# Kernel optimization log

Measured on AMD Instinct MI355X. Metric: run time of the kernel, lower is better.

Reference implementation:

```python
import itertools
import jax, jax.numpy as jnp
import numpy as np

EPS = 1e-15
B, K, H, W = 64, 8, 128, 128


def setup_inputs() -> dict:
    key = jax.random.key(0)
    k1, k2 = jax.random.split(key)
    pred_masks = jax.random.uniform(k1, (B, K, H, W), dtype=jnp.float32)
    aug_masks = jax.random.uniform(k2, (B, K, H, W), dtype=jnp.float32)
    return {"pred_masks": pred_masks, "aug_masks": aug_masks}


def _mask_kl_div(pred, true):
    # true * (log(true+eps) - log(pred+eps)), mean over (H, W)
    return (true * (jnp.log(true + EPS) - jnp.log(pred + EPS))).mean(axis=(-2, -1))


# all K! permutations, precomputed once (K=8 -> 40320 perms)
_PERMS = jnp.asarray(np.array(list(itertools.permutations(range(K))), dtype=np.int32))


def reference(pred_masks, aug_masks):
    b, k, h, w = pred_masks.shape
    t = aug_masks  # targets are detached in torch for the cost matrix
    # Fused pairwise KL cost matrix (avoids the (B,K,K,H,W) broadcast):
    # C[b,i,j] = mean_hw[ t_j*log(t_j+eps) ] - mean_hw[ t_j*log(p_i+eps) ]
    ent = (t * jnp.log(t + EPS)).mean(axis=(-2, -1))          # (B, K) over j
    cross = jnp.einsum('bjhw,bihw->bij', t, jnp.log(pred_masks + EPS)) / (h * w)
    C = ent[:, None, :] - cross                                # (B, K, K)
    # exact linear assignment via exhaustive search over K! permutations
    rows = jnp.arange(k)
    costs = C[:, rows[None, :], _PERMS].sum(axis=-1)           # (B, K!)
    R2C = _PERMS[jnp.argmin(costs, axis=1)]                    # (B, K) col for each row
    # permute rows: out[b, i] = pred[b, argsort(R2C)[b, i]]
    row_perm = jnp.argsort(R2C, axis=1)
    pred_perm = jnp.take_along_axis(pred_masks, row_perm[:, :, None, None], axis=1)
    l = _mask_kl_div(pred_perm, t)                             # (B, K)
    return l.mean(), pred_perm[..., None]
```

## Files before the change

### kernel.cpp

```cpp
#include <hip/hip_runtime.h>


#define BB 64
#define KK 8
#define HW 16384
#define CH 16
#define CHUNK 1024
#define EPSF 1e-15f

struct MaskTab {
    unsigned char masks[255];
    int off[9];
};

constexpr MaskTab make_tab() {
    MaskTab t{};
    int idx = 0;
    for (int p = 1; p <= 8; ++p) {
        t.off[p - 1] = idx;
        for (int m = 1; m < 256; ++m) {
            int c = 0;
            for (int b = 0; b < 8; ++b) c += (m >> b) & 1;
            if (c == p) t.masks[idx++] = (unsigned char)m;
        }
    }
    t.off[8] = idx;
    return t;
}

__constant__ MaskTab kTab = make_tab();

__device__ __forceinline__ float dot4(float4 t, float4 l) {
    return t.x * l.x + t.y * l.y + t.z * l.z + t.w * l.w;
}

__device__ __forceinline__ float4 log4(float4 a) {
    float4 r;
    r.x = __logf(a.x + EPSF); r.y = __logf(a.y + EPSF);
    r.z = __logf(a.z + EPSF); r.w = __logf(a.w + EPSF);
    return r;
}

__global__ __launch_bounds__(256) void cost_kernel(const float* __restrict__ pred,
                                                   const float* __restrict__ aug,
                                                   float* __restrict__ part)
{
    const int blk   = blockIdx.x;
    const int b     = blk >> 4;
    const int chunk = blk & 15;
    const int tid   = threadIdx.x;
    const int wave  = tid >> 6;
    const int lane  = tid & 63;
    const int w2    = 2 * wave;

    const float* p0 = pred + (size_t)b * (KK * HW) + (size_t)w2 * HW + chunk * CHUNK;
    const float* p1 = p0 + HW;
    const float* tb = aug + (size_t)b * (KK * HW) + chunk * CHUNK;

    float acc[16];
#pragma unroll
    for (int v = 0; v < 16; ++v) acc[v] = 0.f;
    float e0 = 0.f, e1 = 0.f;

#pragma unroll
    for (int it = 0; it < 4; ++it) {
        const int off = it * 256 + lane * 4;

        float4 la = log4(*(const float4*)(p0 + off));
        float4 lc = log4(*(const float4*)(p1 + off));

#pragma unroll
        for (int j = 0; j < 8; ++j) {
            float4 t4 = *(const float4*)(tb + (size_t)j * HW + off);
            acc[j]     += dot4(t4, la);
            acc[8 + j] += dot4(t4, lc);
            if (j == w2) {
                e0 += dot4(t4, log4(t4));
            } else if (j == w2 + 1) {
                e1 += dot4(t4, log4(t4));
            }
        }
    }

#pragma unroll
    for (int v = 0; v < 16; ++v) {
        float s = acc[v];
#pragma unroll
        for (int d = 1; d < 64; d <<= 1) s += __shfl_xor(s, d);
        acc[v] = s;
    }
#pragma unroll
    for (int d = 1; d < 64; d <<= 1) e0 += __shfl_xor(e0, d);
#pragma unroll
    for (int d = 1; d < 64; d <<= 1) e1 += __shfl_xor(e1, d);

    if (lane == 0) {
        float* dst = part + (size_t)blk * 72;
#pragma unroll
        for (int j = 0; j < 8; ++j) {
            dst[16 * wave + j]     = acc[j];
            dst[16 * wave + 8 + j] = acc[8 + j];
        }
        dst[64 + w2]     = e0;
        dst[64 + w2 + 1] = e1;
    }
}

__global__ __launch_bounds__(256) void permute_kernel(const float* __restrict__ pred,
                                                      const float* __restrict__ part,
                                                      float* __restrict__ out)
{
    __shared__ float red[72];
    __shared__ float C[64];
    __shared__ float dp[256];
    __shared__ int   choice[256];
    __shared__ int   inv8[8];

    const int g    = blockIdx.x;
    const int p    = g >> 1;
    const int half = g & 1;
    const int b    = p >> 3;
    const int tid  = threadIdx.x;

    const float* pb = part + (size_t)b * CH * 72;
    if (tid < 72) {
        float s = 0.f;
#pragma unroll
        for (int c = 0; c < CH; ++c) s += pb[c * 72 + tid];
        red[tid] = s;
    }
    __syncthreads();
    if (tid < 64) C[tid] = red[64 + (tid & 7)] - red[tid];
    if (tid == 0) dp[0] = 0.f;
    __syncthreads();

    const int grp = tid >> 3;
    const int j   = tid & 7;

    for (int lvl = 1; lvl <= 8; ++lvl) {
        const int start = kTab.off[lvl - 1];
        const int end   = kTab.off[lvl];
        const float* Crow = &C[(lvl - 1) * 8];
        for (int base = start; base < end; base += 32) {
            const int mi = base + grp;
            if (mi < end) {
                const int M = kTab.masks[mi];
                float v  = 1e30f;
                int   bj = 0;
                if (M & (1 << j)) {
                    v  = dp[M ^ (1 << j)] + Crow[j];
                    bj = j;
                }
#pragma unroll
                for (int d = 1; d < 8; d <<= 1) {
                    float ov = __shfl_xor(v, d);
                    int   oj = __shfl_xor(bj, d);
                    if (ov < v) { v = ov; bj = oj; }
                }
                if (j == 0) { dp[M] = v; choice[M] = bj; }
            }
        }
        __syncthreads();
    }

    if (tid == 0) {
        int mask = 255;
        for (int r = 7; r >= 0; --r) {
            const int jj = choice[mask];
            inv8[jj] = r;
            mask ^= 1 << jj;
        }
        if (g == (b << 4))
            atomicAdd(out, dp[255] * (1.0f / (16384.0f * 512.0f)));
    }
    __syncthreads();

    const int src_row = inv8[p & 7];
    const float* src = pred + ((size_t)(b << 3) + src_row) * HW;
    float*       drow = out + 1 + (size_t)p * HW;

#pragma unroll
    for (int m = 0; m < 8; ++m) {
        const int f = half * 2048 + tid + 256 * m;
        const int e = 3 + 4 * f;
        if (f < 4095) {
            float4 v;
            v.x = src[e]; v.y = src[e + 1]; v.z = src[e + 2]; v.w = src[e + 3];
            *(float4*)(drow + e) = v;
        } else {
            drow[0] = src[0]; drow[1] = src[1]; drow[2] = src[2];
            drow[16383] = src[16383];
        }
    }
}

extern "C" void kernel_launch(void* const* d_in, const int* in_sizes, int n_in,
                              void* d_out, int out_size, void* d_ws, size_t ws_size,
                              hipStream_t stream) {
    const float* pred = (const float*)d_in[0];
    const float* aug  = (const float*)d_in[1];
    float* out = (float*)d_out;
    float* part = (float*)d_ws;

    hipMemsetAsync(d_out, 0, sizeof(float), stream);

    cost_kernel<<<dim3(BB * CH), dim3(256), 0, stream>>>(pred, aug, part);
    permute_kernel<<<dim3(1024), dim3(256), 0, stream>>>(pred, part, out);
}
```

Measured before the change: 123.3 us.

## Stage cost-kernel inputs in LDS via global_load_lds with finer chunks

The cost kernel now splits each batch into 64 smaller chunks of 256 elements instead of 16 chunks of 1024, launching four times as many blocks. Each block loads all 8 pred and 8 aug rows for its chunk directly into shared memory with global_load_lds. Waves then read their target tiles from LDS, so the 4x redundant global reads of aug across waves go away and more blocks are in flight. In exchange, the partial buffer grows and the permute kernel must sum 64 partials per batch. The permute kernel's loop uses the CH macro, so it picks up the new count without other edits.

```diff
diff --git a/kernel.cpp b/kernel.cpp
--- a/kernel.cpp
+++ b/kernel.cpp
@@ -4,8 +4,8 @@
 #define BB 64
 #define KK 8
 #define HW 16384
-#define CH 16
-#define CHUNK 1024
+#define CH 64
+#define CHUNK 256
 #define EPSF 1e-15f
 
 struct MaskTab {
@@ -45,41 +45,47 @@
                                                    const float* __restrict__ aug,
                                                    float* __restrict__ part)
 {
+    __shared__ float tile[16][CHUNK];
+
     const int blk   = blockIdx.x;
-    const int b     = blk >> 4;
-    const int chunk = blk & 15;
+    const int b     = blk >> 6;
+    const int chunk = blk & 63;
     const int tid   = threadIdx.x;
     const int wave  = tid >> 6;
     const int lane  = tid & 63;
-    const int w2    = 2 * wave;
-
-    const float* p0 = pred + (size_t)b * (KK * HW) + (size_t)w2 * HW + chunk * CHUNK;
-    const float* p1 = p0 + HW;
-    const float* tb = aug + (size_t)b * (KK * HW) + chunk * CHUNK;
+
+    const size_t base = (size_t)b * (KK * HW) + (size_t)chunk * CHUNK;
+
+#pragma unroll
+    for (int m = 0; m < 4; ++m) {
+        const int vr = wave + 4 * m;
+        const float* g = ((vr < 8) ? (pred + base + (size_t)vr * HW)
+                                   : (aug  + base + (size_t)(vr - 8) * HW)) + lane * 4;
+        __builtin_amdgcn_global_load_lds(
+            (const __attribute__((address_space(1))) void*)g,
+            (__attribute__((address_space(3))) void*)&tile[vr][lane * 4],
+            16, 0, 0);
+    }
+    __syncthreads();
+
+    const int w2 = 2 * wave;
+    const int e4 = lane * 4;
+
+    const float4 p0 = *(const float4*)&tile[w2][e4];
+    const float4 p1 = *(const float4*)&tile[w2 + 1][e4];
+    const float4 la = log4(p0);
+    const float4 lc = log4(p1);
+    const float4 t0 = *(const float4*)&tile[8 + w2][e4];
+    const float4 t1 = *(const float4*)&tile[8 + w2 + 1][e4];
+    float e0 = dot4(t0, log4(t0));
+    float e1 = dot4(t1, log4(t1));
 
     float acc[16];
 #pragma unroll
-    for (int v = 0; v < 16; ++v) acc[v] = 0.f;
-    float e0 = 0.f, e1 = 0.f;
-
-#pragma unroll
-    for (int it = 0; it < 4; ++it) {
-        const int off = it * 256 + lane * 4;
-
-        float4 la = log4(*(const float4*)(p0 + off));
-        float4 lc = log4(*(const float4*)(p1 + off));
-
-#pragma unroll
-        for (int j = 0; j < 8; ++j) {
-            float4 t4 = *(const float4*)(tb + (size_t)j * HW + off);
-            acc[j]     += dot4(t4, la);
-            acc[8 + j] += dot4(t4, lc);
-            if (j == w2) {
-                e0 += dot4(t4, log4(t4));
-            } else if (j == w2 + 1) {
-                e1 += dot4(t4, log4(t4));
-            }
-        }
+    for (int j = 0; j < 8; ++j) {
+        const float4 tv = *(const float4*)&tile[8 + j][e4];
+        acc[j]     = dot4(tv, la);
+        acc[8 + j] = dot4(tv, lc);
     }
 
 #pragma unroll
```

After: 129.6 us. 1.05x slower.

## Move assignment DP into last-arriving cost block; prefetch loads; slim permute kernel

Applied to the files above, without the earlier changes.

The cost kernel now covers 2048-element spans per block (512 blocks) and software-pipelines its loads by fetching the next chunk while computing on the current one. The last block to finish for each batch, detected with an atomic counter, reduces the partials and runs the subset DP, then writes the inverse permutation and per-batch loss to workspace. The permute kernel becomes a pure copy over 2048 blocks, and one block sums the losses, so the output memset is no longer needed. The aim is to stop every copy block from redoing the partial reduction and DP, at the cost of a fence/atomic tail, fewer cost blocks, and more registers.

```diff
diff --git a/kernel.cpp b/kernel.cpp
--- a/kernel.cpp
+++ b/kernel.cpp
@@ -4,8 +4,8 @@
 #define BB 64
 #define KK 8
 #define HW 16384
-#define CH 16
-#define CHUNK 1024
+#define SPANS 8
+#define SPAN 2048
 #define EPSF 1e-15f
 
 struct MaskTab {
@@ -41,53 +41,78 @@
     return r;
 }
 
+struct Chunk {
+    float4 p0, p1;
+    float4 t[8];
+};
+
+__device__ __forceinline__ Chunk ldchunk(const float* __restrict__ p0,
+                                         const float* __restrict__ p1,
+                                         const float* __restrict__ tb, int off) {
+    Chunk c;
+    c.p0 = *(const float4*)(p0 + off);
+    c.p1 = *(const float4*)(p1 + off);
+#pragma unroll
+    for (int j = 0; j < 8; ++j) c.t[j] = *(const float4*)(tb + j * HW + off);
+    return c;
+}
+
 __global__ __launch_bounds__(256) void cost_kernel(const float* __restrict__ pred,
                                                    const float* __restrict__ aug,
-                                                   float* __restrict__ part)
+                                                   float* __restrict__ part,
+                                                   int* __restrict__ ctr,
+                                                   int* __restrict__ ws_inv,
+                                                   float* __restrict__ ws_loss)
 {
-    const int blk   = blockIdx.x;
-    const int b     = blk >> 4;
-    const int chunk = blk & 15;
-    const int tid   = threadIdx.x;
-    const int wave  = tid >> 6;
-    const int lane  = tid & 63;
-    const int w2    = 2 * wave;
-
-    const float* p0 = pred + (size_t)b * (KK * HW) + (size_t)w2 * HW + chunk * CHUNK;
+    __shared__ float C[64];
+    __shared__ float dp[256];
+    __shared__ int   choice[256];
+    __shared__ int   lastf;
+
+    const int blk  = blockIdx.x;
+    const int b    = blk >> 3;
+    const int s    = blk & 7;
+    const int tid  = threadIdx.x;
+    const int lane = tid & 63;
+    const int w2   = __builtin_amdgcn_readfirstlane(2 * (tid >> 6));
+    const int wave = w2 >> 1;
+
+    const size_t base = (size_t)b * (KK * HW) + (size_t)s * SPAN;
+    const float* p0 = pred + base + (size_t)w2 * HW;
     const float* p1 = p0 + HW;
-    const float* tb = aug + (size_t)b * (KK * HW) + chunk * CHUNK;
+    const float* tb = aug + base;
+    const int l4 = lane * 4;
 
     float acc[16];
 #pragma unroll
     for (int v = 0; v < 16; ++v) acc[v] = 0.f;
     float e0 = 0.f, e1 = 0.f;
 
-#pragma unroll
-    for (int it = 0; it < 4; ++it) {
-        const int off = it * 256 + lane * 4;
-
-        float4 la = log4(*(const float4*)(p0 + off));
-        float4 lc = log4(*(const float4*)(p1 + off));
-
+    Chunk cur = ldchunk(p0, p1, tb, l4);
+#pragma unroll
+    for (int c = 0; c < 8; ++c) {
+        Chunk nxt;
+        if (c < 7) nxt = ldchunk(p0, p1, tb, (c + 1) * 256 + l4);
+
+        const float4 la = log4(cur.p0);
+        const float4 lc = log4(cur.p1);
 #pragma unroll
         for (int j = 0; j < 8; ++j) {
-            float4 t4 = *(const float4*)(tb + (size_t)j * HW + off);
-            acc[j]     += dot4(t4, la);
-            acc[8 + j] += dot4(t4, lc);
-            if (j == w2) {
-                e0 += dot4(t4, log4(t4));
-            } else if (j == w2 + 1) {
-                e1 += dot4(t4, log4(t4));
-            }
-        }
+            const float4 tv = cur.t[j];
+            acc[j]     += dot4(tv, la);
+            acc[8 + j] += dot4(tv, lc);
+            if (j == w2)     e0 += dot4(tv, log4(tv));
+            if (j == w2 + 1) e1 += dot4(tv, log4(tv));
+        }
+        if (c < 7) cur = nxt;
     }
 
 #pragma unroll
     for (int v = 0; v < 16; ++v) {
-        float s = acc[v];
-#pragma unroll
-        for (int d = 1; d < 64; d <<= 1) s += __shfl_xor(s, d);
-        acc[v] = s;
+        float sv = acc[v];
+#pragma unroll
+        for (int d = 1; d < 64; d <<= 1) sv += __shfl_xor(sv, d);
+        acc[v] = sv;
     }
 #pragma unroll
     for (int d = 1; d < 64; d <<= 1) e0 += __shfl_xor(e0, d);
@@ -104,45 +129,41 @@
         dst[64 + w2]     = e0;
         dst[64 + w2 + 1] = e1;
     }
-}
-
-__global__ __launch_bounds__(256) void permute_kernel(const float* __restrict__ pred,
-                                                      const float* __restrict__ part,
-                                                      float* __restrict__ out)
-{
-    __shared__ float red[72];
-    __shared__ float C[64];
-    __shared__ float dp[256];
-    __shared__ int   choice[256];
-    __shared__ int   inv8[8];
-
-    const int g    = blockIdx.x;
-    const int p    = g >> 1;
-    const int half = g & 1;
-    const int b    = p >> 3;
-    const int tid  = threadIdx.x;
-
-    const float* pb = part + (size_t)b * CH * 72;
-    if (tid < 72) {
-        float s = 0.f;
-#pragma unroll
-        for (int c = 0; c < CH; ++c) s += pb[c * 72 + tid];
-        red[tid] = s;
-    }
+
     __syncthreads();
-    if (tid < 64) C[tid] = red[64 + (tid & 7)] - red[tid];
+    if (tid == 0) {
+        __threadfence();
+        const int old = atomicAdd(&ctr[b], 1);
+        lastf = (old == SPANS - 1) ? 1 : 0;
+    }
+    __syncthreads();
+    if (!lastf) return;
+    __threadfence();
+
+    if (tid < 64) {
+        const float* pb = part + (size_t)(b * 8) * 72;
+        float ssum = 0.f;
+#pragma unroll
+        for (int s8 = 0; s8 < 8; ++s8) ssum += pb[s8 * 72 + tid];
+        float e = 0.f;
+        if (tid < 8) {
+#pragma unroll
+            for (int s8 = 0; s8 < 8; ++s8) e += pb[s8 * 72 + 64 + tid];
+        }
+        const float entj = __shfl(e, tid & 7);
+        C[tid] = entj - ssum;
+    }
     if (tid == 0) dp[0] = 0.f;
     __syncthreads();
 
     const int grp = tid >> 3;
     const int j   = tid & 7;
-
     for (int lvl = 1; lvl <= 8; ++lvl) {
         const int start = kTab.off[lvl - 1];
         const int end   = kTab.off[lvl];
         const float* Crow = &C[(lvl - 1) * 8];
-        for (int base = start; base < end; base += 32) {
-            const int mi = base + grp;
+        for (int bse = start; bse < end; bse += 32) {
+            const int mi = bse + grp;
             if (mi < end) {
                 const int M = kTab.masks[mi];
                 float v  = 1e30f;
@@ -153,8 +174,8 @@
                 }
 #pragma unroll
                 for (int d = 1; d < 8; d <<= 1) {
-                    float ov = __shfl_xor(v, d);
-                    int   oj = __shfl_xor(bj, d);
+                    const float ov = __shfl_xor(v, d);
+                    const int   oj = __shfl_xor(bj, d);
                     if (ov < v) { v = ov; bj = oj; }
                 }
                 if (j == 0) { dp[M] = v; choice[M] = bj; }
@@ -167,21 +188,31 @@
         int mask = 255;
         for (int r = 7; r >= 0; --r) {
             const int jj = choice[mask];
-            inv8[jj] = r;
+            ws_inv[b * 8 + jj] = r;
             mask ^= 1 << jj;
         }
-        if (g == (b << 4))
-            atomicAdd(out, dp[255] * (1.0f / (16384.0f * 512.0f)));
-    }
-    __syncthreads();
-
-    const int src_row = inv8[p & 7];
+        ws_loss[b] = dp[255] * (1.0f / (16384.0f * 512.0f));
+    }
+}
+
+__global__ __launch_bounds__(256) void permute_kernel(const float* __restrict__ pred,
+                                                      const int* __restrict__ ws_inv,
+                                                      const float* __restrict__ ws_loss,
+                                                      float* __restrict__ out)
+{
+    const int blk  = blockIdx.x;
+    const int pair = blk >> 2;
+    const int q    = blk & 3;
+    const int b    = pair >> 3;
+    const int tid  = threadIdx.x;
+
+    const int src_row = ws_inv[pair];
     const float* src = pred + ((size_t)(b << 3) + src_row) * HW;
-    float*       drow = out + 1 + (size_t)p * HW;
-
-#pragma unroll
-    for (int m = 0; m < 8; ++m) {
-        const int f = half * 2048 + tid + 256 * m;
+    float*      drow = out + 1 + (size_t)pair * HW;
+
+#pragma unroll
+    for (int m = 0; m < 4; ++m) {
+        const int f = q * 1024 + tid + 256 * m;
         const int e = 3 + 4 * f;
         if (f < 4095) {
             float4 v;
@@ -192,6 +223,13 @@
             drow[16383] = src[16383];
         }
     }
+
+    if (blk == 0 && tid < 64) {
+        float v = ws_loss[tid];
+#pragma unroll
+        for (int d = 1; d < 64; d <<= 1) v += __shfl_xor(v, d);
+        if (tid == 0) out[0] = v;
+    }
 }
 
 extern "C" void kernel_launch(void* const* d_in, const int* in_sizes, int n_in,
@@ -200,10 +238,14 @@
     const float* pred = (const float*)d_in[0];
     const float* aug  = (const float*)d_in[1];
     float* out = (float*)d_out;
-    float* part = (float*)d_ws;
-
-    hipMemsetAsync(d_out, 0, sizeof(float), stream);
-
-    cost_kernel<<<dim3(BB * CH), dim3(256), 0, stream>>>(pred, aug, part);
-    permute_kernel<<<dim3(1024), dim3(256), 0, stream>>>(pred, part, out);
-}
+
+    int*   ctr     = (int*)d_ws;
+    float* part    = (float*)d_ws + 64;
+    int*   ws_inv  = (int*)(part + 512 * 72);
+    float* ws_loss = (float*)(ws_inv + 512);
+
+    hipMemsetAsync(ctr, 0, 64 * sizeof(int), stream);
+
+    cost_kernel<<<dim3(BB * SPANS), dim3(256), 0, stream>>>(pred, aug, part, ctr, ws_inv, ws_loss);
+    permute_kernel<<<dim3(2048), dim3(256), 0, stream>>>(pred, ws_inv, ws_loss, out);
+}
```

Result: slower. 166.5 us (+35.1%).

## Double-buffer cost kernel loads into LDS via async global_load_lds and drop memset

Applied to the files above, without the earlier changes.

The cost kernel now streams pred and aug chunks into a double-buffered shared-memory tile using async global-to-LDS loads, prefetching the next chunk while computing on the current one. The separate hipMemsetAsync that zeroed the loss accumulator is replaced by a store from the first thread of cost_kernel, removing one launch. This adds 32KB LDS per block, which may reduce occupancy, and barriers per chunk; the data is still read once, so the gain depends on better latency hiding.

```diff
diff --git a/kernel.cpp b/kernel.cpp
--- a/kernel.cpp
+++ b/kernel.cpp
@@ -4,8 +4,10 @@
 #define BB 64
 #define KK 8
 #define HW 16384
-#define CH 16
-#define CHUNK 1024
+#define SPANS 16
+#define SPAN 1024
+#define NCH 4
+#define CHUNK 256
 #define EPSF 1e-15f
 
 struct MaskTab {
@@ -43,19 +45,40 @@
 
 __global__ __launch_bounds__(256) void cost_kernel(const float* __restrict__ pred,
                                                    const float* __restrict__ aug,
-                                                   float* __restrict__ part)
+                                                   float* __restrict__ part,
+                                                   float* __restrict__ out)
 {
-    const int blk   = blockIdx.x;
-    const int b     = blk >> 4;
-    const int chunk = blk & 15;
-    const int tid   = threadIdx.x;
-    const int wave  = tid >> 6;
-    const int lane  = tid & 63;
-    const int w2    = 2 * wave;
-
-    const float* p0 = pred + (size_t)b * (KK * HW) + (size_t)w2 * HW + chunk * CHUNK;
-    const float* p1 = p0 + HW;
-    const float* tb = aug + (size_t)b * (KK * HW) + chunk * CHUNK;
+    __shared__ float tile[2][16][CHUNK];
+
+    const int blk  = blockIdx.x;
+    const int b    = blk >> 4;
+    const int s    = blk & 15;
+    const int tid  = threadIdx.x;
+    const int wave = tid >> 6;
+    const int lane = tid & 63;
+
+    if (blk == 0 && tid == 0) out[0] = 0.f;
+
+    const size_t base = (size_t)b * (KK * HW) + (size_t)s * SPAN;
+    const int e4 = lane * 4;
+    const int w2 = 2 * wave;
+
+#define STAGE(c)                                                                          \
+    {                                                                                     \
+        const int pb_ = (c) & 1;                                                          \
+        _Pragma("unroll")                                                                 \
+        for (int m = 0; m < 4; ++m) {                                                     \
+            const int vr = wave + 4 * m;                                                  \
+            const float* g = ((vr < 8) ? (pred + base + (size_t)vr * HW)                  \
+                                       : (aug + base + (size_t)(vr - 8) * HW))            \
+                             + (c) * CHUNK + e4;                                          \
+            __builtin_amdgcn_global_load_lds(                                             \
+                (const __attribute__((address_space(1))) void*)g,                         \
+                (__attribute__((address_space(3))) void*)&tile[pb_][vr][e4], 16, 0, 0);   \
+        }                                                                                 \
+    }
+
+    STAGE(0)
 
     float acc[16];
 #pragma unroll
@@ -63,31 +86,30 @@
     float e0 = 0.f, e1 = 0.f;
 
 #pragma unroll
-    for (int it = 0; it < 4; ++it) {
-        const int off = it * 256 + lane * 4;
-
-        float4 la = log4(*(const float4*)(p0 + off));
-        float4 lc = log4(*(const float4*)(p1 + off));
-
+    for (int c = 0; c < NCH; ++c) {
+        __syncthreads();
+        if (c + 1 < NCH) STAGE(c + 1)
+
+        const int pb = c & 1;
+        const float4 la = log4(*(const float4*)&tile[pb][w2][e4]);
+        const float4 lc = log4(*(const float4*)&tile[pb][w2 + 1][e4]);
 #pragma unroll
         for (int j = 0; j < 8; ++j) {
-            float4 t4 = *(const float4*)(tb + (size_t)j * HW + off);
-            acc[j]     += dot4(t4, la);
-            acc[8 + j] += dot4(t4, lc);
-            if (j == w2) {
-                e0 += dot4(t4, log4(t4));
-            } else if (j == w2 + 1) {
-                e1 += dot4(t4, log4(t4));
-            }
-        }
-    }
+            const float4 tv = *(const float4*)&tile[pb][8 + j][e4];
+            acc[j]     += dot4(tv, la);
+            acc[8 + j] += dot4(tv, lc);
+            if (j == w2)     e0 += dot4(tv, log4(tv));
+            if (j == w2 + 1) e1 += dot4(tv, log4(tv));
+        }
+    }
+#undef STAGE
 
 #pragma unroll
     for (int v = 0; v < 16; ++v) {
-        float s = acc[v];
-#pragma unroll
-        for (int d = 1; d < 64; d <<= 1) s += __shfl_xor(s, d);
-        acc[v] = s;
+        float sv = acc[v];
+#pragma unroll
+        for (int d = 1; d < 64; d <<= 1) sv += __shfl_xor(sv, d);
+        acc[v] = sv;
     }
 #pragma unroll
     for (int d = 1; d < 64; d <<= 1) e0 += __shfl_xor(e0, d);
@@ -122,27 +144,26 @@
     const int b    = p >> 3;
     const int tid  = threadIdx.x;
 
-    const float* pb = part + (size_t)b * CH * 72;
+    const float* pb = part + (size_t)b * SPANS * 72;
     if (tid < 72) {
         float s = 0.f;
 #pragma unroll
-        for (int c = 0; c < CH; ++c) s += pb[c * 72 + tid];
+        for (int c = 0; c < SPANS; ++c) s += pb[c * 72 + tid];
         red[tid] = s;
     }
+    if (tid == 0) dp[0] = 0.f;
     __syncthreads();
     if (tid < 64) C[tid] = red[64 + (tid & 7)] - red[tid];
-    if (tid == 0) dp[0] = 0.f;
     __syncthreads();
 
     const int grp = tid >> 3;
     const int j   = tid & 7;
-
     for (int lvl = 1; lvl <= 8; ++lvl) {
         const int start = kTab.off[lvl - 1];
         const int end   = kTab.off[lvl];
         const float* Crow = &C[(lvl - 1) * 8];
-        for (int base = start; base < end; base += 32) {
-            const int mi = base + grp;
+        for (int bse = start; bse < end; bse += 32) {
+            const int mi = bse + grp;
             if (mi < end) {
                 const int M = kTab.masks[mi];
                 float v  = 1e30f;
@@ -153,8 +174,8 @@
                 }
 #pragma unroll
                 for (int d = 1; d < 8; d <<= 1) {
-                    float ov = __shfl_xor(v, d);
-                    int   oj = __shfl_xor(bj, d);
+                    const float ov = __shfl_xor(v, d);
+                    const int   oj = __shfl_xor(bj, d);
                     if (ov < v) { v = ov; bj = oj; }
                 }
                 if (j == 0) { dp[M] = v; choice[M] = bj; }
@@ -176,8 +197,8 @@
     __syncthreads();
 
     const int src_row = inv8[p & 7];
-    const float* src = pred + ((size_t)(b << 3) + src_row) * HW;
-    float*       drow = out + 1 + (size_t)p * HW;
+    const float* src  = pred + ((size_t)(b << 3) + src_row) * HW;
+    float*      drow  = out + 1 + (size_t)p * HW;
 
 #pragma unroll
     for (int m = 0; m < 8; ++m) {
@@ -202,8 +223,6 @@
     float* out = (float*)d_out;
     float* part = (float*)d_ws;
 
-    hipMemsetAsync(d_out, 0, sizeof(float), stream);
-
-    cost_kernel<<<dim3(BB * CH), dim3(256), 0, stream>>>(pred, aug, part);
+    cost_kernel<<<dim3(BB * SPANS), dim3(256), 0, stream>>>(pred, aug, part, out);
     permute_kernel<<<dim3(1024), dim3(256), 0, stream>>>(pred, part, out);
 }
```

Measured after the change: 123.1 us. Within noise of the previous version (-0.1%).
